# Kernel tuning notes

Measured on AMD Instinct MI355X. Metric: run time of the kernel, lower is better.

Reference implementation:

```python
import jax, jax.numpy as jnp
import numpy as np

NUM_SPECIES = 4
NUM_PAIRS = NUM_SPECIES * (NUM_SPECIES + 1) // 2  # 10 species pairs
RCR = 5.2   # radial cutoff (Angstrom)
RCA = 3.5   # angular cutoff (must be < RCR)
ETA_R = 16.0
SHF_R = jnp.asarray(0.9 + 0.26875 * np.arange(16), dtype=jnp.float32)
ETA_A = 8.0
ZETA = 32.0
SHF_A = jnp.asarray(0.9 + 0.65 * np.arange(4), dtype=jnp.float32)       # 4 angular radial shifts
SHF_Z = jnp.asarray((np.pi / 16.0) * (1.0 + 2.0 * np.arange(8)), dtype=jnp.float32)  # 8 angle sections


def _triu_index(num_species):
    # mirrors AEVComputer._calculate_triu_index
    s1, s2 = np.triu_indices(num_species, 0)
    ret = np.zeros((num_species, num_species), dtype=np.int32)
    ret[s1, s2] = np.arange(len(s1))
    ret[s2, s1] = np.arange(len(s1))
    return jnp.asarray(ret)

TRIU = _triu_index(NUM_SPECIES)


def _fc(d, rc):
    # cosine cutoff; the (d <= rc) validity is applied via masks outside
    return 0.5 * jnp.cos(jnp.pi * d / rc) + 0.5


def _aev(species, coords):
    N, A = species.shape
    dt = coords.dtype
    diff = coords[:, None, :, :] - coords[:, :, None, :]          # (N,i,j,3): r_j - r_i
    eye = jnp.eye(A, dtype=bool)
    d2 = jnp.sum(diff * diff, axis=-1)
    dist = jnp.sqrt(jnp.where(eye, 1.0, d2))                      # (N,i,j), self-distance guarded

    # ---- radial AEV: 0.25 * exp(-EtaR*(d-ShfR)^2) * fc(d), scattered by neighbor species ----
    rmask = (~eye) & (dist <= RCR)
    rad = 0.25 * jnp.exp(-ETA_R * (dist[..., None] - SHF_R) ** 2) * _fc(dist, RCR)[..., None]
    rad = rad * rmask[..., None].astype(dt)                       # (N,i,j,16)
    sp1h = jax.nn.one_hot(species, NUM_SPECIES, dtype=dt)         # (N,j,S)
    radial_aev = jnp.einsum('nijr,njs->nisr', rad, sp1h).reshape(N, A, -1)  # (N,A,64)

    # ---- angular AEV over triples (i; j,k), j,k neighbors of i within RCA ----
    amask = (~eye) & (dist <= RCA)                                # (N,i,j)
    tri = amask[:, :, :, None] & amask[:, :, None, :] & (~eye)[None, None]  # (N,i,j,k), j!=k
    dot = jnp.einsum('nijc,nikc->nijk', diff, diff)
    cos = 0.95 * dot / (dist[:, :, :, None] * dist[:, :, None, :])  # 0.95 stabilizer as in torchani
    theta = jnp.arccos(jnp.clip(cos, -0.95, 0.95))                # (N,i,j,k)
    fcj = _fc(dist, RCA)
    base = 2.0 * fcj[:, :, :, None] * fcj[:, :, None, :] * tri.astype(dt)
    davg = 0.5 * (dist[:, :, :, None] + dist[:, :, None, :])
    f2 = jnp.exp(-ETA_A * (davg[..., None] - SHF_A) ** 2)         # (N,i,j,k,ShfA=4)
    f1 = ((1.0 + jnp.cos(theta[..., None] - SHF_Z)) * 0.5) ** ZETA  # (N,i,j,k,ShfZ=8)
    term = (base[..., None, None] * f2[..., :, None] * f1[..., None, :]).reshape(N, A, A, A, -1)
    pair_idx = TRIU[species[:, :, None], species[:, None, :]]     # (N,j,k)
    pair1h = jax.nn.one_hot(pair_idx, NUM_PAIRS, dtype=dt)        # (N,j,k,P=10)
    # each unordered pair {j,k} is counted once in torchani -> 0.5 * symmetric ordered sum
    angular_aev = 0.5 * jnp.einsum('nijkq,njkp->nipq', term, pair1h).reshape(N, A, -1)  # (N,A,320)

    return jnp.concatenate([radial_aev, angular_aev], axis=-1)    # (N,A,384)


def setup_inputs():
    key = jax.random.key(0)
    k1, k2 = jax.random.split(key)
    N, A, BOX = 16, 64, 12.0
    coords = jax.random.uniform(k1, (N, A, 3), dtype=jnp.float32) * BOX  # atoms in a 12 A box
    species = jax.random.randint(k2, (N, A), 0, NUM_SPECIES)
    return {"species": species, "coords": coords}


def reference(species, coords):
    # SpeciesAEV: (species, aev) with aev shape (N, A, aev_length=384)
    return species, _aev(species, coords)
```

## Files before the change

### kernel.cpp

```cpp
#include <hip/hip_runtime.h>

#define RCR 5.2f
#define RCA 3.5f
#define PI_F 3.14159265358979323846f

__constant__ int c_triu[16] = {0,1,2,3, 1,4,5,6, 2,5,7,8, 3,6,8,9};

__global__ __launch_bounds__(64) void aev_kernel(
    const int* __restrict__ species,
    const float* __restrict__ coords,
    float* __restrict__ out,
    int NA)
{
    const int blk = blockIdx.x;
    const int n   = blk >> 6;
    const int i   = blk & 63;
    const int tid = threadIdx.x;

    __shared__ float sx[64], sy[64], sz[64];
    __shared__ int   ssp[64];
    __shared__ float dxs[64], dys[64], dzs[64], ds[64];
    __shared__ float aev[384];
    __shared__ int   nbr[64];
    __shared__ int   nbr_count;

    const float* c = coords + (size_t)(n * 64) * 3;
    sx[tid]  = c[tid * 3 + 0];
    sy[tid]  = c[tid * 3 + 1];
    sz[tid]  = c[tid * 3 + 2];
    ssp[tid] = species[n * 64 + tid];
    for (int f = tid; f < 384; f += 64) aev[f] = 0.0f;
    if (tid == 0) nbr_count = 0;
    __syncthreads();

    const float xi = sx[i], yi = sy[i], zi = sz[i];
    const float ddx = sx[tid] - xi;
    const float ddy = sy[tid] - yi;
    const float ddz = sz[tid] - zi;
    const float d2  = ddx * ddx + ddy * ddy + ddz * ddz;
    const float d   = sqrtf(d2);
    dxs[tid] = ddx; dys[tid] = ddy; dzs[tid] = ddz; ds[tid] = d;

    const bool isj = (tid != i);

    if (isj && d <= RCR) {
        const float fc  = 0.5f * cosf((PI_F / RCR) * d) + 0.5f;
        const float pre = 0.25f * fc;
        const int   base = ssp[tid] * 16;
        #pragma unroll
        for (int r = 0; r < 16; r++) {
            const float t = d - (0.9f + 0.26875f * (float)r);
            atomicAdd(&aev[base + r], pre * expf(-16.0f * t * t));
        }
    }

    if (isj && d <= RCA) {
        const int idx = atomicAdd(&nbr_count, 1);
        nbr[idx] = tid;
    }
    __syncthreads();

    const int M = nbr_count;
    for (int q = tid; q < M * M; q += 64) {
        const int jj = q / M;
        const int kk = q - jj * M;
        if (kk <= jj) continue;
        const int j = nbr[jj], k = nbr[kk];
        const float dij = ds[j], dik = ds[k];
        const float dot = dxs[j] * dxs[k] + dys[j] * dys[k] + dzs[j] * dzs[k];
        float cosv = 0.95f * dot / (dij * dik);
        cosv = fminf(0.95f, fmaxf(-0.95f, cosv));
        const float theta = acosf(cosv);
        const float fcij  = 0.5f * cosf((PI_F / RCA) * dij) + 0.5f;
        const float fcik  = 0.5f * cosf((PI_F / RCA) * dik) + 0.5f;
        const float base2 = 2.0f * fcij * fcik;
        const float davg  = 0.5f * (dij + dik);
        const int   pidx  = c_triu[ssp[j] * 4 + ssp[k]];
        float f2[4];
        #pragma unroll
        for (int a = 0; a < 4; a++) {
            const float t = davg - (0.9f + 0.65f * (float)a);
            f2[a] = base2 * expf(-8.0f * t * t);
        }
        float* dst = &aev[64 + pidx * 32];
        #pragma unroll
        for (int z = 0; z < 8; z++) {
            const float tz = (1.0f + cosf(theta - (PI_F / 16.0f) * (1.0f + 2.0f * (float)z))) * 0.5f;
            const float t2  = tz * tz;
            const float t4  = t2 * t2;
            const float t8  = t4 * t4;
            const float t16 = t8 * t8;
            const float t32 = t16 * t16;
            #pragma unroll
            for (int a = 0; a < 4; a++) {
                atomicAdd(&dst[a * 8 + z], f2[a] * t32);
            }
        }
    }
    __syncthreads();

    const int atom = n * 64 + i;
    if (tid == 0) out[atom] = (float)ssp[i];
    float* dstg = out + NA + (size_t)atom * 384;
    for (int f = tid; f < 384; f += 64) dstg[f] = aev[f];
}

extern "C" void kernel_launch(void* const* d_in, const int* in_sizes, int n_in,
                              void* d_out, int out_size, void* d_ws, size_t ws_size,
                              hipStream_t stream) {
    const int*   species = (const int*)d_in[0];
    const float* coords  = (const float*)d_in[1];
    float*       out     = (float*)d_out;
    const int NA = in_sizes[0];
    aev_kernel<<<NA, 64, 0, stream>>>(species, coords, out, NA);
}
```

Before: 65.78 us.

## Replace shared-memory atomics with per-thread output ownership and trig identity

Each thread now owns fixed output features (one radial, five angular) and loops over all neighbors or pairs, accumulating in registers instead of doing shared-memory atomicAdds. The angular cosine term uses cos(theta-phi)=cos*cosphi+sin*sinphi, which removes acos and cos calls per pair. The neighbor list is built with a wavefront ballot and popcount instead of atomics, and fast intrinsics (__expf, __cosf, __frcp_rn) replace the precise math calls. The trade-off is redundant work: every thread evaluates every pair serially (M^2/2 iterations with 5 exps each) and discards the results whose species pair does not match, and the fast intrinsics reduce accuracy slightly.

Result: slower. 76.05 us (+15.6%).

```diff
diff --git a/kernel.cpp b/kernel.cpp
--- a/kernel.cpp
+++ b/kernel.cpp
@@ -20,89 +20,101 @@
     __shared__ float sx[64], sy[64], sz[64];
     __shared__ int   ssp[64];
     __shared__ float dxs[64], dys[64], dzs[64], ds[64];
-    __shared__ float aev[384];
+    __shared__ float pre_r[64];
+    __shared__ float fca[64];
     __shared__ int   nbr[64];
-    __shared__ int   nbr_count;
 
     const float* c = coords + (size_t)(n * 64) * 3;
     sx[tid]  = c[tid * 3 + 0];
     sy[tid]  = c[tid * 3 + 1];
     sz[tid]  = c[tid * 3 + 2];
     ssp[tid] = species[n * 64 + tid];
-    for (int f = tid; f < 384; f += 64) aev[f] = 0.0f;
-    if (tid == 0) nbr_count = 0;
     __syncthreads();
 
     const float xi = sx[i], yi = sy[i], zi = sz[i];
     const float ddx = sx[tid] - xi;
     const float ddy = sy[tid] - yi;
     const float ddz = sz[tid] - zi;
-    const float d2  = ddx * ddx + ddy * ddy + ddz * ddz;
-    const float d   = sqrtf(d2);
+    const float d   = sqrtf(ddx * ddx + ddy * ddy + ddz * ddz);
     dxs[tid] = ddx; dys[tid] = ddy; dzs[tid] = ddz; ds[tid] = d;
 
     const bool isj = (tid != i);
+    pre_r[tid] = (isj && d <= RCR)
+                   ? 0.25f * (0.5f * __cosf((PI_F / RCR) * d) + 0.5f) : 0.0f;
+    fca[tid]   = 0.5f * __cosf((PI_F / RCA) * d) + 0.5f;
 
-    if (isj && d <= RCR) {
-        const float fc  = 0.5f * cosf((PI_F / RCR) * d) + 0.5f;
-        const float pre = 0.25f * fc;
-        const int   base = ssp[tid] * 16;
-        #pragma unroll
-        for (int r = 0; r < 16; r++) {
-            const float t = d - (0.9f + 0.26875f * (float)r);
-            atomicAdd(&aev[base + r], pre * expf(-16.0f * t * t));
-        }
+    const bool apred = isj && (d <= RCA);
+    const unsigned long long bal = __ballot(apred);
+    if (apred) {
+        const int pos = __popcll(bal & ((1ull << tid) - 1ull));
+        nbr[pos] = tid;
+    }
+    const int M = __popcll(bal);
+    __syncthreads();
+
+    const int   my_s   = tid >> 4;
+    const float my_shf = 0.9f + 0.26875f * (float)(tid & 15);
+    float racc = 0.0f;
+    #pragma unroll 4
+    for (int j = 0; j < 64; j++) {
+        const float t = ds[j] - my_shf;
+        const float e = pre_r[j] * __expf(-16.0f * t * t);
+        racc += (ssp[j] == my_s) ? e : 0.0f;
     }
 
-    if (isj && d <= RCA) {
-        const int idx = atomicAdd(&nbr_count, 1);
-        nbr[idx] = tid;
+    float acc[5];
+    int   my_p[5];
+    float my_shfa[5], my_cphi[5], my_sphi[5];
+    #pragma unroll
+    for (int u = 0; u < 5; u++) {
+        const int b = tid + 64 * u;
+        my_p[u] = b >> 5;
+        const int a = (b >> 3) & 3;
+        const int z = b & 7;
+        my_shfa[u] = 0.9f + 0.65f * (float)a;
+        const float phi = (PI_F / 16.0f) * (float)(1 + 2 * z);
+        float sp_, cp_;
+        __sincosf(phi, &sp_, &cp_);
+        my_cphi[u] = cp_;
+        my_sphi[u] = sp_;
+        acc[u] = 0.0f;
     }
-    __syncthreads();
 
-    const int M = nbr_count;
-    for (int q = tid; q < M * M; q += 64) {
-        const int jj = q / M;
-        const int kk = q - jj * M;
-        if (kk <= jj) continue;
-        const int j = nbr[jj], k = nbr[kk];
-        const float dij = ds[j], dik = ds[k];
-        const float dot = dxs[j] * dxs[k] + dys[j] * dys[k] + dzs[j] * dzs[k];
-        float cosv = 0.95f * dot / (dij * dik);
-        cosv = fminf(0.95f, fmaxf(-0.95f, cosv));
-        const float theta = acosf(cosv);
-        const float fcij  = 0.5f * cosf((PI_F / RCA) * dij) + 0.5f;
-        const float fcik  = 0.5f * cosf((PI_F / RCA) * dik) + 0.5f;
-        const float base2 = 2.0f * fcij * fcik;
-        const float davg  = 0.5f * (dij + dik);
-        const int   pidx  = c_triu[ssp[j] * 4 + ssp[k]];
-        float f2[4];
-        #pragma unroll
-        for (int a = 0; a < 4; a++) {
-            const float t = davg - (0.9f + 0.65f * (float)a);
-            f2[a] = base2 * expf(-8.0f * t * t);
-        }
-        float* dst = &aev[64 + pidx * 32];
-        #pragma unroll
-        for (int z = 0; z < 8; z++) {
-            const float tz = (1.0f + cosf(theta - (PI_F / 16.0f) * (1.0f + 2.0f * (float)z))) * 0.5f;
-            const float t2  = tz * tz;
-            const float t4  = t2 * t2;
-            const float t8  = t4 * t4;
-            const float t16 = t8 * t8;
-            const float t32 = t16 * t16;
+    for (int jj = 1; jj < M; jj++) {
+        const int j = nbr[jj];
+        const float dij = ds[j];
+        const float xj = dxs[j], yj = dys[j], zj = dzs[j];
+        const float fcj = fca[j];
+        const int sj4 = ssp[j] * 4;
+        for (int kk = 0; kk < jj; kk++) {
+            const int k = nbr[kk];
+            const float dik = ds[k];
+            const float dot = xj * dxs[k] + yj * dys[k] + zj * dzs[k];
+            float cosv = 0.95f * dot * __frcp_rn(dij * dik);
+            cosv = fminf(0.95f, fmaxf(-0.95f, cosv));
+            const float sinv = sqrtf(1.0f - cosv * cosv);
+            const float base2 = 2.0f * fcj * fca[k];
+            const float davg  = 0.5f * (dij + dik);
+            const int   pidx  = c_triu[sj4 + ssp[k]];
             #pragma unroll
-            for (int a = 0; a < 4; a++) {
-                atomicAdd(&dst[a * 8 + z], f2[a] * t32);
+            for (int u = 0; u < 5; u++) {
+                const float t  = davg - my_shfa[u];
+                const float e  = base2 * __expf(-8.0f * t * t);
+                const float w  = cosv * my_cphi[u] + sinv * my_sphi[u];
+                const float tz = 0.5f + 0.5f * w;
+                const float t2 = tz * tz, t4 = t2 * t2, t8 = t4 * t4;
+                const float t16 = t8 * t8, t32 = t16 * t16;
+                acc[u] += (pidx == my_p[u]) ? e * t32 : 0.0f;
             }
         }
     }
-    __syncthreads();
 
     const int atom = n * 64 + i;
     if (tid == 0) out[atom] = (float)ssp[i];
     float* dstg = out + NA + (size_t)atom * 384;
-    for (int f = tid; f < 384; f += 64) dstg[f] = aev[f];
+    dstg[tid] = racc;
+    #pragma unroll
+    for (int u = 0; u < 5; u++) dstg[64 + tid + 64 * u] = acc[u];
 }
 
 extern "C" void kernel_launch(void* const* d_in, const int* in_sizes, int n_in,
```
